# Kernel optimization log

Measured on AMD Instinct MI355X. Metric: run time of the kernel, lower is better.

## Reference

```python
import jax, jax.numpy as jnp
import numpy as np

N_PHENO = 50000
N_GENE = 50000
H = 128
N_LAYERS = 3  # num_layers=2 hidden convs + 1 final conv


def _seg_mean(x_src, edge, n_dst):
    # mean aggregation of source features onto destination nodes (PyG SAGEConv default)
    msg = x_src[edge[0]]                       # [E, H] gather
    s = jax.ops.segment_sum(msg, edge[1], num_segments=n_dst)
    cnt = jax.ops.segment_sum(jnp.ones((edge.shape[1],), x_src.dtype), edge[1], num_segments=n_dst)
    return s / jnp.maximum(cnt, 1.0)[:, None]


def _sage(x_src, x_dst, edge, Wl, bl, Wr, n_dst):
    # SAGEConv: lin_l(mean_j x_j) + lin_r(x_i); lin_l has bias, lin_r does not
    return _seg_mean(x_src, edge, n_dst) @ Wl + bl + x_dst @ Wr


def setup_inputs() -> dict:
    key = jax.random.key(0)
    ks = jax.random.split(key, 16)
    d = {
        'x_pheno': jax.random.normal(ks[0], (N_PHENO, H), jnp.float32),
        'x_gene': jax.random.normal(ks[1], (N_GENE, H), jnp.float32),
    }
    scale = 1.0 / np.sqrt(H)
    names = ['Wl_isa', 'bl_isa', 'Wr_isa', 'Wl_rel', 'bl_rel', 'Wr_rel', 'Wl_rev', 'bl_rev', 'Wr_rev']
    for i, nm in enumerate(names):
        shp = (N_LAYERS, H) if nm.startswith('b') else (N_LAYERS, H, H)
        d[nm] = jax.random.normal(ks[2 + i], shp, jnp.float32) * scale
    d['edge_isa'] = jax.random.randint(ks[11], (2, 500000), 0, N_PHENO, jnp.int64)
    d['edge_rel'] = jax.random.randint(ks[12], (2, 1000000), 0, N_GENE, jnp.int64)
    d['edge_rev'] = jax.random.randint(ks[13], (2, 1000000), 0, N_PHENO, jnp.int64)
    d['edge_label_index'] = jax.random.randint(ks[14], (2, 500000), 0, N_PHENO, jnp.int64)
    return d


def reference(x_pheno, x_gene, Wl_isa, bl_isa, Wr_isa, Wl_rel, bl_rel, Wr_rel,
              Wl_rev, bl_rev, Wr_rev, edge_isa, edge_rel, edge_rev, edge_label_index):
    xp, xg = x_pheno, x_gene
    n_p, n_g = xp.shape[0], xg.shape[0]
    for i in range(N_LAYERS):
        # HeteroConv aggr='sum': sum SAGE outputs across edge types per dst node type
        new_p = (_sage(xp, xp, edge_isa, Wl_isa[i], bl_isa[i], Wr_isa[i], n_p)
                 + _sage(xg, xp, edge_rev, Wl_rev[i], bl_rev[i], Wr_rev[i], n_p))
        new_g = _sage(xp, xg, edge_rel, Wl_rel[i], bl_rel[i], Wr_rel[i], n_g)
        if i < N_LAYERS - 1:  # leaky_relu after hidden convs, not after `final`
            new_p = jax.nn.leaky_relu(new_p, 0.01)
            new_g = jax.nn.leaky_relu(new_g, 0.01)
        xp, xg = new_p, new_g
    # Classifier: dot-product edge decoder + sigmoid
    score = (xp[edge_label_index[0]] * xg[edge_label_index[1]]).sum(axis=-1)
    return jax.nn.sigmoid(score)
```

## Files before the change

kernel.cpp:

```cpp
#include <hip/hip_runtime.h>
#include <hip/hip_bf16.h>
#include <math.h>

#define H 128
#define RS 136
#define BSH 9
#define BINW 512
#define BCAP 11264
#define BSLOT 12288
#define KEDGE 4096
#define EPT 16
#define MAXBINS 1024

typedef __attribute__((ext_vector_type(8))) short short8;
typedef __attribute__((ext_vector_type(4))) short short4v;
typedef __attribute__((ext_vector_type(2))) short short2v;
typedef __attribute__((ext_vector_type(4))) float f32x4;
typedef __attribute__((ext_vector_type(2))) _Float16 half2v;
typedef __attribute__((ext_vector_type(4))) _Float16 half4v;
typedef __attribute__((ext_vector_type(8))) _Float16 half8v;

__device__ __forceinline__ short f2bf(float f) {
    unsigned u = __float_as_uint(f);
    u += 0x7fff + ((u >> 16) & 1);
    return (short)(u >> 16);
}
__device__ __forceinline__ float bf2f(short h) {
    return __uint_as_float(((unsigned)(unsigned short)h) << 16);
}


__global__ __launch_bounds__(256) void bin_scatter_kernel(
    const int* __restrict__ e0, int E0, const int* __restrict__ e1, int E1,
    const int* __restrict__ e2, int E2, int* __restrict__ bin_cur,
    int* __restrict__ temp, int NPn, int NGn, int nbins, int E_tot) {
    __shared__ int hist[MAXBINS];
    __shared__ int cur[MAXBINS];
    int t = threadIdx.x;
    for (int i = t; i < nbins; i += 256) hist[i] = 0;
    __syncthreads();
    int vals[EPT], bins[EPT];
    int base_e = blockIdx.x * KEDGE;
#pragma unroll
    for (int j = 0; j < EPT; ++j) {
        int g = base_e + j * 256 + t;
        int b = -1, v = 0;
        if (g < E_tot) {
            const int* ed; int E, lo, nbase;
            if (g < E0) { ed = e0; E = E0; lo = g; nbase = 0; }
            else if (g < E0 + E1) { ed = e1; E = E1; lo = g - E0; nbase = NPn; }
            else { ed = e2; E = E2; lo = g - E0 - E1; nbase = NPn + NGn; }
            int src = ed[lo];
            int gdst = nbase + ed[E + lo];
            v = src | ((gdst & (BINW - 1)) << 16);
            b = gdst >> BSH;
            atomicAdd(&hist[b], 1);
        }
        vals[j] = v;
        bins[j] = b;
    }
    __syncthreads();
    for (int i = t; i < nbins; i += 256) {
        int h = hist[i];
        cur[i] = h ? atomicAdd(&bin_cur[i * 16], h) : 0;
    }
    __syncthreads();
#pragma unroll
    for (int j = 0; j < EPT; ++j) {
        if (bins[j] >= 0) {
            int p = atomicAdd(&cur[bins[j]], 1);
            if (p < BSLOT) temp[(size_t)bins[j] * BSLOT + p] = vals[j];
        }
    }
}

__global__ __launch_bounds__(1024) void scan_bins(const int* __restrict__ bin_cur, int nbins,
                                                  int* __restrict__ bin_base) {
    __shared__ int sh[1024];
    int t = threadIdx.x;
    int v = 0;
    if (t < nbins) { v = bin_cur[t * 16]; if (v > BSLOT) v = BSLOT; }
    sh[t] = v;
    __syncthreads();
    for (int off = 1; off < 1024; off <<= 1) {
        int u = (t >= off) ? sh[t - off] : 0;
        __syncthreads();
        sh[t] += u;
        __syncthreads();
    }
    if (t < nbins) bin_base[t] = sh[t] - v;
    if (t == nbins - 1) bin_base[nbins] = sh[t];
}

__global__ __launch_bounds__(256) void bin_sort_kernel(
    const int* __restrict__ bin_base, const int* __restrict__ temp,
    int* __restrict__ col, int* __restrict__ rowptr, int n_tot, int nbins) {
    __shared__ int srt[BCAP];
    __shared__ int cur[BINW];
    __shared__ int pfx[BINW];
    __shared__ int red[256];
    int b = blockIdx.x;
    int start = b << BSH;
    int nodes = n_tot - start; if (nodes > BINW) nodes = BINW;
    int t = threadIdx.x;
    int base = bin_base[b];
    int count = bin_base[b + 1] - base;
    const int* __restrict__ tb = temp + (size_t)b * BSLOT;
    for (int i = t; i < BINW; i += 256) cur[i] = 0;
    __syncthreads();
    for (int i = t; i < count; i += 256)
        atomicAdd(&cur[(tb[i] >> 16) & (BINW - 1)], 1);
    __syncthreads();
    int a0 = cur[2 * t], a1 = cur[2 * t + 1];
    red[t] = a0 + a1;
    __syncthreads();
    for (int off = 1; off < 256; off <<= 1) {
        int u = (t >= off) ? red[t - off] : 0;
        __syncthreads();
        red[t] += u;
        __syncthreads();
    }
    int excl = red[t] - (a0 + a1);
    pfx[2 * t] = excl;
    pfx[2 * t + 1] = excl + a0;
    __syncthreads();
    for (int i = t; i < nodes; i += 256) rowptr[start + i] = base + pfx[i];
    if (b == nbins - 1 && t == 0) rowptr[n_tot] = base + count;
    for (int i = t; i < BINW; i += 256) cur[i] = pfx[i];
    __syncthreads();
    if (count <= BCAP) {
        for (int i = t; i < count; i += 256) {
            int v = tb[i];
            int p = atomicAdd(&cur[(v >> 16) & (BINW - 1)], 1);
            srt[p] = v & 0xFFFF;
        }
        __syncthreads();
        for (int i = t; i < count; i += 256) col[base + i] = srt[i];
    } else {
        for (int i = t; i < count; i += 256) {
            int v = tb[i];
            int p = atomicAdd(&cur[(v >> 16) & (BINW - 1)], 1);
            col[base + p] = v & 0xFFFF;
        }
    }
}


struct WSrc { const float* a[15]; const float* b[15]; };

__global__ __launch_bounds__(256) void pack_w_kernel(WSrc src, short* __restrict__ whi,
                                                     short* __restrict__ wlo) {
    int idx = blockIdx.x * 256 + threadIdx.x;
    if (idx >= 15 * 4 * 8 * 64) return;
    int lane = idx & 63;
    int ct = (idx >> 6) & 7;
    int kc = (idx >> 9) & 3;
    int mat = idx >> 11;
    const float* A = src.a[mat];
    const float* Bp = src.b[mat];
    int n = ct * 16 + (lane & 15);
    int kbase = kc * 32 + (lane >> 4) * 8;
    size_t o = (size_t)idx * 8;
    for (int j = 0; j < 8; ++j) {
        float v = A[(size_t)(kbase + j) * H + n];
        if (Bp) v += Bp[(size_t)(kbase + j) * H + n];
        short h = f2bf(v);
        whi[o + j] = h;
        wlo[o + j] = f2bf(v - bf2f(h));
    }
}


__global__ __launch_bounds__(256) void cvt16_kernel(const float* __restrict__ xa, int n4a,
                                                    const float* __restrict__ xb, int n4b,
                                                    _Float16* __restrict__ ya,
                                                    _Float16* __restrict__ yb) {
    int i = blockIdx.x * 256 + threadIdx.x;
    const float* x; _Float16* y;
    if (i < n4a) { x = xa + (size_t)i * 4; y = ya + (size_t)i * 4; }
    else if (i < n4a + n4b) { x = xb + (size_t)(i - n4a) * 4; y = yb + (size_t)(i - n4a) * 4; }
    else return;
    f32x4 v = *(const f32x4*)x;
    half4v h;
#pragma unroll
    for (int k = 0; k < 4; ++k) h[k] = (_Float16)v[k];
    *(half4v*)y = h;
}


__device__ __forceinline__ float2 seg16(const _Float16* __restrict__ x,
                                        const int* __restrict__ rowptr,
                                        const int* __restrict__ col,
                                        int rb, int voff) {
    int beg = rowptr[rb], end = rowptr[rb + 1];
    float ax0 = 0.f, ax1 = 0.f, ax2 = 0.f, ax3 = 0.f;
    float ay0 = 0.f, ay1 = 0.f, ay2 = 0.f, ay3 = 0.f;
    int e = beg;
    while (e + 16 <= end) {
        half2v v[16];
#pragma unroll
        for (int i = 0; i < 16; ++i) {
            int si = __builtin_amdgcn_readfirstlane(col[e + i]);
            v[i] = *(const half2v*)(x + (size_t)si * H + voff);
        }
#pragma unroll
        for (int i = 0; i < 16; i += 4) {
            ax0 += (float)v[i + 0][0]; ay0 += (float)v[i + 0][1];
            ax1 += (float)v[i + 1][0]; ay1 += (float)v[i + 1][1];
            ax2 += (float)v[i + 2][0]; ay2 += (float)v[i + 2][1];
            ax3 += (float)v[i + 3][0]; ay3 += (float)v[i + 3][1];
        }
        e += 16;
    }
    int rem = end - e;
    if (rem > 8) {
        int last = end - 1;
        half2v v[16];
#pragma unroll
        for (int i = 0; i < 16; ++i) {
            int p = e + i; if (p > last) p = last;
            int si = __builtin_amdgcn_readfirstlane(col[p]);
            v[i] = *(const half2v*)(x + (size_t)si * H + voff);
        }
#pragma unroll
        for (int i = 0; i < 16; ++i) {
            float m = (i < rem) ? 1.0f : 0.0f;
            float fx = (float)v[i][0], fy = (float)v[i][1];
            if ((i & 3) == 0) { ax0 = fmaf(fx, m, ax0); ay0 = fmaf(fy, m, ay0); }
            else if ((i & 3) == 1) { ax1 = fmaf(fx, m, ax1); ay1 = fmaf(fy, m, ay1); }
            else if ((i & 3) == 2) { ax2 = fmaf(fx, m, ax2); ay2 = fmaf(fy, m, ay2); }
            else { ax3 = fmaf(fx, m, ax3); ay3 = fmaf(fy, m, ay3); }
        }
    } else if (rem > 0) {
        int last = end - 1;
        half2v v[8];
#pragma unroll
        for (int i = 0; i < 8; ++i) {
            int p = e + i; if (p > last) p = last;
            int si = __builtin_amdgcn_readfirstlane(col[p]);
            v[i] = *(const half2v*)(x + (size_t)si * H + voff);
        }
#pragma unroll
        for (int i = 0; i < 8; ++i) {
            float m = (i < rem) ? 1.0f : 0.0f;
            float fx = (float)v[i][0], fy = (float)v[i][1];
            if ((i & 3) == 0) { ax0 = fmaf(fx, m, ax0); ay0 = fmaf(fy, m, ay0); }
            else if ((i & 3) == 1) { ax1 = fmaf(fx, m, ax1); ay1 = fmaf(fy, m, ay1); }
            else if ((i & 3) == 2) { ax2 = fmaf(fx, m, ax2); ay2 = fmaf(fy, m, ay2); }
            else { ax3 = fmaf(fx, m, ax3); ay3 = fmaf(fy, m, ay3); }
        }
    }
    float sx = (ax0 + ax1) + (ax2 + ax3);
    float sy = (ay0 + ay1) + (ay2 + ay3);
    int c = end - beg; if (c < 1) c = 1;
    float inv = 1.0f / (float)c;
    return (float2){sx * inv, sy * inv};
}


struct GTerm {
    const _Float16* x;
    int rbase;
    const short* hi;
    const short* lo;
    const float* f;
};

template <int NIN>
__device__ __forceinline__ void layer_body(
    short* __restrict__ Ahi, short* __restrict__ Alo,
    GTerm t0, GTerm t1, GTerm t2,
    const int* __restrict__ rowptr, const int* __restrict__ col,
    const short* __restrict__ whi, const short* __restrict__ wlo,
    int mat0, int mat1, int mat2,
    const float* __restrict__ b0, const float* __restrict__ b1,
    _Float16* __restrict__ out16, short* __restrict__ ohi, short* __restrict__ olo,
    int n_rows, int relu, int bx) {
    const int tid = threadIdx.x;
    const int lane = tid & 63;
    const int wave = __builtin_amdgcn_readfirstlane(tid >> 6);
    const int r0 = bx * 64;
    const int ct0 = wave * 2;
    const int m16 = lane & 15;
    const int acol = (lane >> 4) * 8;

    f32x4 acc[4][2];
#pragma unroll
    for (int mt = 0; mt < 4; ++mt)
#pragma unroll
        for (int c = 0; c < 2; ++c) acc[mt][c] = (f32x4){0.f, 0.f, 0.f, 0.f};

    const GTerm terms[3] = {t0, t1, t2};
    const int marr[3] = {mat0, mat1, mat2};

#pragma unroll
    for (int m = 0; m < NIN; ++m) {
        const GTerm& T = terms[m];
        __syncthreads();
        if (T.x) {
            int voff = lane * 2;
            for (int rr = 0; rr < 16; ++rr) {
                int lrow = wave * 16 + rr;
                int gr = r0 + lrow;
                if (gr >= n_rows) gr = n_rows - 1;
                float2 s = seg16(T.x, rowptr, col, T.rbase + gr, voff);
                short h0 = f2bf(s.x), h1 = f2bf(s.y);
                *(short2v*)&Ahi[lrow * RS + voff] = (short2v){h0, h1};
                *(short2v*)&Alo[lrow * RS + voff] =
                    (short2v){f2bf(s.x - bf2f(h0)), f2bf(s.y - bf2f(h1))};
            }
        } else if (T.hi) {
#pragma unroll
            for (int i = 0; i < 8; ++i) {
                int f = tid + i * 256;
                int row = f >> 5;
                int c4 = (f & 31) * 4;
                int gr = r0 + row;
                if (gr >= n_rows) gr = n_rows - 1;
                size_t o = (size_t)gr * H + c4;
                *(short4v*)&Ahi[row * RS + c4] = *(const short4v*)&T.hi[o];
                *(short4v*)&Alo[row * RS + c4] = *(const short4v*)&T.lo[o];
            }
        } else {
            const float* __restrict__ A = T.f;
#pragma unroll
            for (int i = 0; i < 8; ++i) {
                int f = tid + i * 256;
                int row = f >> 5;
                int c4 = (f & 31) * 4;
                int gr = r0 + row;
                if (gr >= n_rows) gr = n_rows - 1;
                float4 v = *(const float4*)&A[(size_t)gr * H + c4];
                short h0 = f2bf(v.x), h1 = f2bf(v.y), h2 = f2bf(v.z), h3 = f2bf(v.w);
                *(short4v*)&Ahi[row * RS + c4] = (short4v){h0, h1, h2, h3};
                *(short4v*)&Alo[row * RS + c4] =
                    (short4v){f2bf(v.x - bf2f(h0)), f2bf(v.y - bf2f(h1)),
                              f2bf(v.z - bf2f(h2)), f2bf(v.w - bf2f(h3))};
            }
        }
        __syncthreads();
        const short* __restrict__ wh = whi + (size_t)marr[m] * (H * H);
        const short* __restrict__ wl = wlo + (size_t)marr[m] * (H * H);
        short8 bh[2][2], bl[2][2];
        {
            size_t f0 = ((size_t)ct0 * 64 + lane) * 8;
            bh[0][0] = *(const short8*)&wh[f0];
            bh[0][1] = *(const short8*)&wh[f0 + 512];
            bl[0][0] = *(const short8*)&wl[f0];
            bl[0][1] = *(const short8*)&wl[f0 + 512];
        }
#pragma unroll
        for (int kc = 0; kc < 4; ++kc) {
            if (kc < 3) {
                int nb = (kc + 1) & 1;
                size_t f = ((size_t)((kc + 1) * 8 + ct0) * 64 + lane) * 8;
                bh[nb][0] = *(const short8*)&wh[f];
                bh[nb][1] = *(const short8*)&wh[f + 512];
                bl[nb][0] = *(const short8*)&wl[f];
                bl[nb][1] = *(const short8*)&wl[f + 512];
            }
            int cb = kc & 1;
#pragma unroll
            for (int mt = 0; mt < 4; ++mt) {
                short8 ah = *(const short8*)&Ahi[(mt * 16 + m16) * RS + kc * 32 + acol];
                short8 al = *(const short8*)&Alo[(mt * 16 + m16) * RS + kc * 32 + acol];
#pragma unroll
                for (int c = 0; c < 2; ++c) {
                    acc[mt][c] = __builtin_amdgcn_mfma_f32_16x16x32_bf16(ah, bh[cb][c], acc[mt][c], 0, 0, 0);
                    acc[mt][c] = __builtin_amdgcn_mfma_f32_16x16x32_bf16(al, bh[cb][c], acc[mt][c], 0, 0, 0);
                    acc[mt][c] = __builtin_amdgcn_mfma_f32_16x16x32_bf16(ah, bl[cb][c], acc[mt][c], 0, 0, 0);
                }
            }
        }
    }

    const int rquad = (lane >> 4) * 4;
    const int ncol = lane & 15;
#pragma unroll
    for (int c = 0; c < 2; ++c) {
        int n = (ct0 + c) * 16 + ncol;
        float bs = b0[n];
        if (b1) bs += b1[n];
#pragma unroll
        for (int mt = 0; mt < 4; ++mt) {
#pragma unroll
            for (int reg = 0; reg < 4; ++reg) {
                int gr = r0 + mt * 16 + rquad + reg;
                if (gr < n_rows) {
                    float v = acc[mt][c][reg] + bs;
                    if (relu) v = v > 0.f ? v : 0.01f * v;
                    size_t o = (size_t)gr * H + n;
                    out16[o] = (_Float16)v;
                    short h = f2bf(v);
                    ohi[o] = h;
                    olo[o] = f2bf(v - bf2f(h));
                }
            }
        }
    }
}

struct LayerArgs {
    GTerm p0, p1, p2, g0, g1;
    const int* rowptr; const int* col;
    const short* whi; const short* wlo;
    int pm0, pm1, pm2, gm0, gm1;
    const float* pb0; const float* pb1; const float* gb0;
    _Float16* pout16; short* poh; short* pol; int np;
    _Float16* gout16; short* goh; short* gol; int ng;
    int relu; int nbp;
};

__global__ __launch_bounds__(256, 3) void fused_layer(LayerArgs a) {
    __shared__ short Ahi[64 * RS];
    __shared__ short Alo[64 * RS];
    int bx = blockIdx.x;
    if (bx < a.nbp) {
        layer_body<3>(Ahi, Alo, a.p0, a.p1, a.p2, a.rowptr, a.col, a.whi, a.wlo,
                      a.pm0, a.pm1, a.pm2, a.pb0, a.pb1,
                      a.pout16, a.poh, a.pol, a.np, a.relu, bx);
    } else {
        layer_body<2>(Ahi, Alo, a.g0, a.g1, a.g1, a.rowptr, a.col, a.whi, a.wlo,
                      a.gm0, a.gm1, 0, a.gb0, nullptr,
                      a.gout16, a.goh, a.gol, a.ng, a.relu, bx - a.nbp);
    }
}


__global__ __launch_bounds__(256) void scores_kernel(const _Float16* __restrict__ xp,
                                                     const _Float16* __restrict__ xg,
                                                     const int* __restrict__ eli, int E,
                                                     float* __restrict__ out) {
    int lane16 = threadIdx.x & 15;
    int sub = threadIdx.x >> 4;
    int e = blockIdx.x * 16 + sub;
    if (e >= E) return;
    int ip = eli[e];
    int ig = eli[E + e];
    half8v a = *(const half8v*)&xp[(size_t)ip * H + lane16 * 8];
    half8v b = *(const half8v*)&xg[(size_t)ig * H + lane16 * 8];
    float s = 0.f;
#pragma unroll
    for (int k = 0; k < 8; ++k) s += (float)a[k] * (float)b[k];
#pragma unroll
    for (int off = 8; off; off >>= 1) s += __shfl_xor(s, off, 16);
    if (lane16 == 0) out[e] = 1.0f / (1.0f + expf(-s));
}


extern "C" void kernel_launch(void* const* d_in, const int* in_sizes, int n_in,
                              void* d_out, int out_size, void* d_ws, size_t ws_size,
                              hipStream_t stream) {
    const float* x_pheno = (const float*)d_in[0];
    const float* x_gene  = (const float*)d_in[1];
    const float* Wl_isa  = (const float*)d_in[2];
    const float* bl_isa  = (const float*)d_in[3];
    const float* Wr_isa  = (const float*)d_in[4];
    const float* Wl_rel  = (const float*)d_in[5];
    const float* bl_rel  = (const float*)d_in[6];
    const float* Wr_rel  = (const float*)d_in[7];
    const float* Wl_rev  = (const float*)d_in[8];
    const float* bl_rev  = (const float*)d_in[9];
    const float* Wr_rev  = (const float*)d_in[10];
    const int* e_isa = (const int*)d_in[11];
    const int* e_rel = (const int*)d_in[12];
    const int* e_rev = (const int*)d_in[13];
    const int* e_lbl = (const int*)d_in[14];
    const int E_isa = in_sizes[11] / 2;
    const int E_rel = in_sizes[12] / 2;
    const int E_rev = in_sizes[13] / 2;
    const int E_lbl = in_sizes[14] / 2;
    const int NP = in_sizes[0] / H;
    const int NG = in_sizes[1] / H;
    const int n_tot = NP + NG + NP;
    const int E_tot = E_isa + E_rel + E_rev;
    const int nbins = (n_tot + BINW - 1) / BINW;

    char* ws = (char*)d_ws;
    auto alloc = [&](size_t bytes) -> char* {
        char* p = ws;
        ws += (bytes + 255) & ~(size_t)255;
        return p;
    };
    int* rowptr  = (int*)alloc((size_t)(n_tot + 1) * 4);
    int* col     = (int*)alloc((size_t)E_tot * 4);
    int* temp    = (int*)alloc((size_t)nbins * BSLOT * 4);
    int* bin_cur = (int*)alloc((size_t)nbins * 16 * 4);
    int* bin_base= (int*)alloc((size_t)(nbins + 1) * 4);
    short* whi = (short*)alloc((size_t)15 * H * H * sizeof(short));
    short* wlo = (short*)alloc((size_t)15 * H * H * sizeof(short));
    _Float16* xpm[2], *xgm[2];
    xpm[0] = (_Float16*)alloc((size_t)NP * H * sizeof(_Float16));
    xpm[1] = (_Float16*)alloc((size_t)NP * H * sizeof(_Float16));
    xgm[0] = (_Float16*)alloc((size_t)NG * H * sizeof(_Float16));
    xgm[1] = (_Float16*)alloc((size_t)NG * H * sizeof(_Float16));
    short* xph = (short*)alloc((size_t)NP * H * sizeof(short));
    short* xpl = (short*)alloc((size_t)NP * H * sizeof(short));
    short* xgh = (short*)alloc((size_t)NG * H * sizeof(short));
    short* xgl = (short*)alloc((size_t)NG * H * sizeof(short));

    hipMemsetAsync(bin_cur, 0, (size_t)nbins * 16 * 4, stream);
    bin_scatter_kernel<<<(E_tot + KEDGE - 1) / KEDGE, 256, 0, stream>>>(
        e_isa, E_isa, e_rel, E_rel, e_rev, E_rev, bin_cur, temp, NP, NG, nbins, E_tot);
    scan_bins<<<1, 1024, 0, stream>>>(bin_cur, nbins, bin_base);
    bin_sort_kernel<<<nbins, 256, 0, stream>>>(bin_base, temp, col, rowptr, n_tot, nbins);

    WSrc src;
    for (int l = 0; l < 3; ++l) {
        src.a[l * 5 + 0] = Wl_isa + (size_t)l * H * H;  src.b[l * 5 + 0] = nullptr;
        src.a[l * 5 + 1] = Wl_rev + (size_t)l * H * H;  src.b[l * 5 + 1] = nullptr;
        src.a[l * 5 + 2] = Wr_isa + (size_t)l * H * H;  src.b[l * 5 + 2] = Wr_rev + (size_t)l * H * H;
        src.a[l * 5 + 3] = Wl_rel + (size_t)l * H * H;  src.b[l * 5 + 3] = nullptr;
        src.a[l * 5 + 4] = Wr_rel + (size_t)l * H * H;  src.b[l * 5 + 4] = nullptr;
    }
    pack_w_kernel<<<(15 * 4 * 8 * 64 + 255) / 256, 256, 0, stream>>>(src, whi, wlo);

    cvt16_kernel<<<((NP + NG) * 32 + 255) / 256, 256, 0, stream>>>(
        x_pheno, NP * 32, x_gene, NG * 32, xpm[0], xgm[0]);

    const short *pph = nullptr, *ppl = nullptr, *pgh = nullptr, *pgl = nullptr;
    const int nbp = (NP + 63) / 64, nbg = (NG + 63) / 64;
    for (int l = 0; l < 3; ++l) {
        int rs = l & 1;
        int wsid = rs ^ 1;
        LayerArgs a;
        a.p0 = GTerm{xpm[rs], 0, nullptr, nullptr, nullptr};
        a.p1 = GTerm{xgm[rs], NP + NG, nullptr, nullptr, nullptr};
        a.p2 = GTerm{nullptr, 0, pph, ppl, l == 0 ? x_pheno : nullptr};
        a.g0 = GTerm{xpm[rs], NP, nullptr, nullptr, nullptr};
        a.g1 = GTerm{nullptr, 0, pgh, pgl, l == 0 ? x_gene : nullptr};
        a.rowptr = rowptr; a.col = col; a.whi = whi; a.wlo = wlo;
        a.pm0 = l * 5 + 0; a.pm1 = l * 5 + 1; a.pm2 = l * 5 + 2;
        a.gm0 = l * 5 + 3; a.gm1 = l * 5 + 4;
        a.pb0 = bl_isa + (size_t)l * H; a.pb1 = bl_rev + (size_t)l * H;
        a.gb0 = bl_rel + (size_t)l * H;
        a.pout16 = xpm[wsid]; a.poh = xph; a.pol = xpl; a.np = NP;
        a.gout16 = xgm[wsid]; a.goh = xgh; a.gol = xgl; a.ng = NG;
        a.relu = (l < 2) ? 1 : 0; a.nbp = nbp;
        fused_layer<<<nbp + nbg, 256, 0, stream>>>(a);
        pph = xph; ppl = xpl; pgh = xgh; pgl = xgl;
    }

    scores_kernel<<<(E_lbl + 15) / 16, 256, 0, stream>>>(xpm[1], xgm[1], e_lbl, E_lbl,
                                                         (float*)d_out);
}
```

Before: 606.1 us.

## Stage block neighbor indices in LDS and gather two rows per pass

In the fused mean-aggregation plus GEMM kernel, the column indices for a 64-row block's CSR range are preloaded into LDS, reusing the Alo buffer, and each wave then aggregates two destination rows at once with 16-deep gather batches. This cuts repeated global index loads and doubles the number of in-flight feature gathers to hide latency. The low-part results are held in registers until the index buffer is free, and blocks whose edge count exceeds the LDS capacity fall back to the old per-row path. The cost is higher register pressure and wasted lanes when the two rows have very different degrees.

```diff
diff --git a/kernel.cpp b/kernel.cpp
--- a/kernel.cpp
+++ b/kernel.cpp
@@ -11,6 +11,7 @@
 #define KEDGE 4096
 #define EPT 16
 #define MAXBINS 1024
+#define IDXCAP 4352
 
 typedef __attribute__((ext_vector_type(8))) short short8;
 typedef __attribute__((ext_vector_type(4))) short short4v;
@@ -299,15 +300,104 @@
         __syncthreads();
         if (T.x) {
             int voff = lane * 2;
-            for (int rr = 0; rr < 16; ++rr) {
-                int lrow = wave * 16 + rr;
-                int gr = r0 + lrow;
-                if (gr >= n_rows) gr = n_rows - 1;
-                float2 s = seg16(T.x, rowptr, col, T.rbase + gr, voff);
-                short h0 = f2bf(s.x), h1 = f2bf(s.y);
-                *(short2v*)&Ahi[lrow * RS + voff] = (short2v){h0, h1};
-                *(short2v*)&Alo[lrow * RS + voff] =
-                    (short2v){f2bf(s.x - bf2f(h0)), f2bf(s.y - bf2f(h1))};
+            int row_end = r0 + 64; if (row_end > n_rows) row_end = n_rows;
+            int beg_blk = rowptr[T.rbase + r0];
+            int tcnt = rowptr[T.rbase + row_end] - beg_blk;
+            if (tcnt > 0 && tcnt <= IDXCAP) {
+                int* lidx = (int*)Alo;
+                for (int i = tid; i < tcnt; i += 256) lidx[i] = col[beg_blk + i];
+                __syncthreads();
+                short2v lo_sm[16];
+#pragma unroll
+                for (int pp = 0; pp < 8; ++pp) {
+                    int gr0 = r0 + wave * 16 + pp * 2;
+                    int gr1 = gr0 + 1;
+                    if (gr0 >= n_rows) gr0 = n_rows - 1;
+                    if (gr1 >= n_rows) gr1 = n_rows - 1;
+                    int rb0 = T.rbase + gr0, rb1 = T.rbase + gr1;
+                    int gb0 = rowptr[rb0], ge0 = rowptr[rb0 + 1];
+                    int gb1 = rowptr[rb1], ge1 = rowptr[rb1 + 1];
+                    int c0 = ge0 - gb0, c1 = ge1 - gb1;
+                    int lb0 = gb0 - beg_blk, lb1 = gb1 - beg_blk;
+                    int ll0 = (c0 > 0) ? lb0 + c0 - 1 : 0;
+                    int ll1 = (c1 > 0) ? lb1 + c1 - 1 : 0;
+                    int cm = c0 > c1 ? c0 : c1;
+                    int mc = (cm + 15) >> 4;
+                    float ax0 = 0.f, ax1 = 0.f, ax2 = 0.f, ax3 = 0.f;
+                    float ay0 = 0.f, ay1 = 0.f, ay2 = 0.f, ay3 = 0.f;
+                    float bx0 = 0.f, bx1 = 0.f, bx2 = 0.f, bx3 = 0.f;
+                    float by0 = 0.f, by1 = 0.f, by2 = 0.f, by3 = 0.f;
+                    for (int c = 0; c < mc; ++c) {
+                        int s0[16], s1[16];
+#pragma unroll
+                        for (int i = 0; i < 16; ++i) {
+                            int q = lb0 + c * 16 + i; if (q > ll0) q = ll0;
+                            s0[i] = lidx[q];
+                        }
+#pragma unroll
+                        for (int i = 0; i < 16; ++i) {
+                            int q = lb1 + c * 16 + i; if (q > ll1) q = ll1;
+                            s1[i] = lidx[q];
+                        }
+                        half2v v0[16], v1[16];
+#pragma unroll
+                        for (int i = 0; i < 16; ++i) {
+                            int u = __builtin_amdgcn_readfirstlane(s0[i]);
+                            v0[i] = *(const half2v*)(T.x + (size_t)u * H + voff);
+                        }
+#pragma unroll
+                        for (int i = 0; i < 16; ++i) {
+                            int u = __builtin_amdgcn_readfirstlane(s1[i]);
+                            v1[i] = *(const half2v*)(T.x + (size_t)u * H + voff);
+                        }
+                        int re0 = c0 - c * 16, re1 = c1 - c * 16;
+#pragma unroll
+                        for (int i = 0; i < 16; ++i) {
+                            float m0 = (i < re0) ? 1.0f : 0.0f;
+                            float m1 = (i < re1) ? 1.0f : 0.0f;
+                            float fx0 = (float)v0[i][0], fy0 = (float)v0[i][1];
+                            float fx1 = (float)v1[i][0], fy1 = (float)v1[i][1];
+                            if ((i & 3) == 0) { ax0 = fmaf(fx0, m0, ax0); ay0 = fmaf(fy0, m0, ay0);
+                                                bx0 = fmaf(fx1, m1, bx0); by0 = fmaf(fy1, m1, by0); }
+                            else if ((i & 3) == 1) { ax1 = fmaf(fx0, m0, ax1); ay1 = fmaf(fy0, m0, ay1);
+                                                     bx1 = fmaf(fx1, m1, bx1); by1 = fmaf(fy1, m1, by1); }
+                            else if ((i & 3) == 2) { ax2 = fmaf(fx0, m0, ax2); ay2 = fmaf(fy0, m0, ay2);
+                                                     bx2 = fmaf(fx1, m1, bx2); by2 = fmaf(fy1, m1, by2); }
+                            else { ax3 = fmaf(fx0, m0, ax3); ay3 = fmaf(fy0, m0, ay3);
+                                   bx3 = fmaf(fx1, m1, bx3); by3 = fmaf(fy1, m1, by3); }
+                        }
+                    }
+                    int d0 = c0 < 1 ? 1 : c0, d1 = c1 < 1 ? 1 : c1;
+                    float i0 = 1.0f / (float)d0, i1 = 1.0f / (float)d1;
+                    float sx0 = ((ax0 + ax1) + (ax2 + ax3)) * i0;
+                    float sy0 = ((ay0 + ay1) + (ay2 + ay3)) * i0;
+                    float sx1 = ((bx0 + bx1) + (bx2 + bx3)) * i1;
+                    float sy1 = ((by0 + by1) + (by2 + by3)) * i1;
+                    int lr0 = wave * 16 + pp * 2;
+                    short h00 = f2bf(sx0), h01 = f2bf(sy0);
+                    short h10 = f2bf(sx1), h11 = f2bf(sy1);
+                    *(short2v*)&Ahi[lr0 * RS + voff] = (short2v){h00, h01};
+                    *(short2v*)&Ahi[(lr0 + 1) * RS + voff] = (short2v){h10, h11};
+                    lo_sm[pp * 2] = (short2v){f2bf(sx0 - bf2f(h00)), f2bf(sy0 - bf2f(h01))};
+                    lo_sm[pp * 2 + 1] = (short2v){f2bf(sx1 - bf2f(h10)), f2bf(sy1 - bf2f(h11))};
+                }
+                __syncthreads();
+#pragma unroll
+                for (int rr = 0; rr < 16; ++rr) {
+                    int lrow = wave * 16 + rr;
+                    *(short2v*)&Alo[lrow * RS + voff] = lo_sm[rr];
+                }
+            } else {
+                for (int rr = 0; rr < 16; ++rr) {
+                    int lrow = wave * 16 + rr;
+                    int gr = r0 + lrow;
+                    if (gr >= n_rows) gr = n_rows - 1;
+                    float2 s = seg16(T.x, rowptr, col, T.rbase + gr, voff);
+                    short h0 = f2bf(s.x), h1 = f2bf(s.y);
+                    *(short2v*)&Ahi[lrow * RS + voff] = (short2v){h0, h1};
+                    *(short2v*)&Alo[lrow * RS + voff] =
+                        (short2v){f2bf(s.x - bf2f(h0)), f2bf(s.y - bf2f(h1))};
+                }
             }
         } else if (T.hi) {
 #pragma unroll
```

Result: slower. 800.7 us (+32.1%).
